# Kernel tuning notes

Measured on AMD Instinct MI355X. Metric: run time of the kernel, lower is better.

The kernel has to match this reference:

```python
import jax, jax.numpy as jnp
import numpy as np

D_MODEL = 256; D_FLOW = 128; D_FFN = 1024
N_HEADS = 8; N_LEVELS = 3; N_POINTS = 4
D_HEAD = D_MODEL // N_HEADS
SHAPES = np.array([[128, 128], [64, 64], [32, 32]], dtype=np.int64)


def setup_inputs():
    key = jax.random.key(0)
    ks = jax.random.split(key, 12)
    N = 2
    LeNin = int((SHAPES[:, 0] * SHAPES[:, 1]).sum())
    Lq = int(SHAPES[0, 0] * SHAPES[0, 1])
    lsi = np.concatenate([[0], np.cumsum(SHAPES[:, 0] * SHAPES[:, 1])[:-1]])
    s = 0.02
    return {
        'src': jax.random.normal(ks[0], (N, LeNin, D_MODEL), jnp.float32),
        'flow': jax.random.normal(ks[1], (N, Lq, D_FLOW), jnp.float32),
        'spatial_shapes': jnp.asarray(SHAPES, jnp.int32),
        'level_start_index': jnp.asarray(lsi, jnp.int32),
        'w_value': jax.random.normal(ks[2], (D_MODEL, D_MODEL), jnp.float32) * s,
        'b_value': jnp.zeros((D_MODEL,), jnp.float32),
        'w_off': jax.random.normal(ks[3], (D_FLOW, N_HEADS * N_LEVELS * N_POINTS * 2), jnp.float32) * s,
        'b_off': jax.random.normal(ks[4], (N_HEADS * N_LEVELS * N_POINTS * 2,), jnp.float32) * 0.5,
        'w_attn': jax.random.normal(ks[5], (D_FLOW, N_HEADS * N_LEVELS * N_POINTS), jnp.float32) * s,
        'b_attn': jnp.zeros((N_HEADS * N_LEVELS * N_POINTS,), jnp.float32),
        'w_out': jax.random.normal(ks[6], (D_MODEL, D_MODEL), jnp.float32) * s,
        'b_out': jnp.zeros((D_MODEL,), jnp.float32),
        'gamma': jnp.ones((D_MODEL,), jnp.float32),
        'beta': jnp.zeros((D_MODEL,), jnp.float32),
        'w1': jax.random.normal(ks[7], (D_MODEL, D_FFN), jnp.float32) * s,
        'b1': jnp.zeros((D_FFN,), jnp.float32),
        'w2': jax.random.normal(ks[8], (D_FFN, D_MODEL), jnp.float32) * s,
        'b2': jnp.zeros((D_MODEL,), jnp.float32),
    }


def _bilinear_level(v, xy, H, W):
    # v: [N, nh, H*W, dh]; xy: [N, Lq, nh, np, 2] normalized to [0,1]
    # grid_sample(align_corners=False) semantics: pixel = loc * size - 0.5, zero padding
    N, Lq = xy.shape[0], xy.shape[1]
    x = xy[..., 0] * W - 0.5
    y = xy[..., 1] * H - 0.5
    x0 = jnp.floor(x); y0 = jnp.floor(y)
    dx = x - x0; dy = y - y0
    acc = jnp.zeros((N, N_HEADS, Lq * N_POINTS, v.shape[-1]), v.dtype)
    corners = ((x0, y0, (1 - dx) * (1 - dy)),
               (x0 + 1, y0, dx * (1 - dy)),
               (x0, y0 + 1, (1 - dx) * dy),
               (x0 + 1, y0 + 1, dx * dy))
    for ix, iy, w in corners:
        valid = (ix >= 0) & (ix <= W - 1) & (iy >= 0) & (iy <= H - 1)
        xi = jnp.clip(ix, 0, W - 1).astype(jnp.int32)
        yi = jnp.clip(iy, 0, H - 1).astype(jnp.int32)
        idx = (yi * W + xi).transpose(0, 2, 1, 3).reshape(N, N_HEADS, Lq * N_POINTS)
        g = jnp.take_along_axis(v, idx[..., None], axis=2)  # [N, nh, Lq*np, dh]
        wv = (w * valid).transpose(0, 2, 1, 3).reshape(N, N_HEADS, Lq * N_POINTS, 1)
        acc = acc + wv * g
    return acc


def reference(src, flow, spatial_shapes, level_start_index, w_value, b_value,
              w_off, b_off, w_attn, b_attn, w_out, b_out, gamma, beta, w1, b1, w2, b2):
    ss = np.asarray(jax.device_get(spatial_shapes))
    lsi = np.asarray(jax.device_get(level_start_index))
    N, LeNin, _ = src.shape
    Lq = flow.shape[1]
    value = (src @ w_value + b_value).reshape(N, LeNin, N_HEADS, D_HEAD)
    off = (flow @ w_off + b_off).reshape(N, Lq, N_HEADS, N_LEVELS, N_POINTS, 2)
    attn = jax.nn.softmax((flow @ w_attn + b_attn).reshape(N, Lq, N_HEADS, N_LEVELS * N_POINTS), axis=-1)
    attn = attn.reshape(N, Lq, N_HEADS, N_LEVELS, N_POINTS)
    # reference points on level-0 grid (valid_ratios == 1)
    H0, W0 = int(ss[0, 0]), int(ss[0, 1])
    ry, rx = jnp.meshgrid(jnp.linspace(0.5, H0 - 0.5, H0) / H0,
                          jnp.linspace(0.5, W0 - 0.5, W0) / W0, indexing='ij')
    ref = jnp.stack([rx.reshape(-1), ry.reshape(-1)], -1)  # [Lq, 2] (x, y)
    norm = jnp.asarray(np.stack([ss[:, 1], ss[:, 0]], -1), jnp.float32)  # [nl, 2] = (W, H)
    loc = ref[None, :, None, None, None, :] + off / norm[None, None, None, :, None, :]
    acc = jnp.zeros((N, Lq, N_HEADS, D_HEAD), src.dtype)
    for l in range(N_LEVELS):
        H, W = int(ss[l, 0]), int(ss[l, 1])
        st = int(lsi[l])
        v = value[:, st:st + H * W].transpose(0, 2, 1, 3)  # [N, nh, HW, dh]
        s_l = _bilinear_level(v, loc[:, :, :, l], H, W).reshape(N, N_HEADS, Lq, N_POINTS, D_HEAD)
        acc = acc + jnp.einsum('bhqpd,bqhp->bqhd', s_l, attn[:, :, :, l])
    src2 = acc.reshape(N, Lq, D_MODEL) @ w_out + b_out
    x = src2  # dropout is identity at inference
    mu = x.mean(-1, keepdims=True)
    var = ((x - mu) ** 2).mean(-1, keepdims=True)
    ln = (x - mu) / jnp.sqrt(var + 1e-5) * gamma + beta
    ffn = jax.nn.relu(ln @ w1 + b1) @ w2 + b2
    return x + ffn
```

## Files before the change

kernel.cpp:

```cpp
#include <hip/hip_runtime.h>
#include <cstdint>
#include <cstddef>

#define D_MODEL  256
#define D_FLOW   128
#define D_FFN    1024
#define N_HEADS  8
#define N_LEVELS 3
#define N_POINTS 4
#define D_HEAD   32
#define LQ       16384
#define LENIN    21504
#define NB       2

typedef unsigned short ushort;
typedef __attribute__((ext_vector_type(8))) short bf16x8;
typedef __attribute__((ext_vector_type(4))) float f32x4;

__device__ __forceinline__ ushort f2b(float f) {
    uint32_t u = __float_as_uint(f);
    uint32_t r = (u + 0x7fffu + ((u >> 16) & 1u)) >> 16;
    return (ushort)r;
}

__device__ __forceinline__ void gl_lds16(const void* g, void* l) {
    __builtin_amdgcn_global_load_lds(
        (const __attribute__((address_space(1))) unsigned int*)g,
        (__attribute__((address_space(3))) unsigned int*)l,
        16, 0, 0);
}

template<bool A_FP32, bool RELU, bool RESID, bool OUT_BF16>
__global__ __launch_bounds__(256)
void mfma_gemm(const void* __restrict__ Ain, const ushort* __restrict__ Bt,
               const float* __restrict__ bias, const float* __restrict__ resid,
               void* __restrict__ Cout, int N, int K)
{
    __shared__ ushort As[128 * 64];
    __shared__ ushort Bs[128 * 64];

    const int tid  = threadIdx.x;
    const int wave = tid >> 6;
    const int lane = tid & 63;
    const int quad = lane >> 4;
    const int l16  = lane & 15;
    const int wr   = (wave >> 1) * 64;
    const int wc   = (wave & 1) * 64;
    const int bm   = blockIdx.y * 128;
    const int bn   = blockIdx.x * 128;

    const int sr  = lane >> 3;
    const int sc  = lane & 7;
    const int gch = sc ^ sr;

    f32x4 acc[4][4] = {};
    const int swz = l16 & 7;

    for (int k0 = 0; k0 < K; k0 += 64) {
        __syncthreads();
        if (A_FP32) {
            const float* Af = (const float*)Ain;
#pragma unroll
            for (int i = 0; i < 4; ++i) {
                const int row = wave * 32 + i * 8 + sr;
                const float* p = Af + (size_t)(bm + row) * K + k0 + gch * 8;
                const float4 v0 = *(const float4*)(p);
                const float4 v1 = *(const float4*)(p + 4);
                bf16x8 pk;
                pk[0] = (short)f2b(v0.x); pk[1] = (short)f2b(v0.y);
                pk[2] = (short)f2b(v0.z); pk[3] = (short)f2b(v0.w);
                pk[4] = (short)f2b(v1.x); pk[5] = (short)f2b(v1.y);
                pk[6] = (short)f2b(v1.z); pk[7] = (short)f2b(v1.w);
                *(bf16x8*)&As[(size_t)row * 64 + sc * 8] = pk;
            }
        } else {
            const ushort* Ab = (const ushort*)Ain;
#pragma unroll
            for (int i = 0; i < 4; ++i) {
                const int row = wave * 32 + i * 8;
                gl_lds16(Ab + (size_t)(bm + row + sr) * K + k0 + gch * 8,
                         As + (size_t)row * 64);
            }
        }
#pragma unroll
        for (int i = 0; i < 4; ++i) {
            const int row = wave * 32 + i * 8;
            gl_lds16(Bt + (size_t)(bn + row + sr) * K + k0 + gch * 8,
                     Bs + (size_t)row * 64);
        }
        __syncthreads();

#pragma unroll
        for (int kk = 0; kk < 2; ++kk) {
            bf16x8 af[4], bfr[4];
#pragma unroll
            for (int mi = 0; mi < 4; ++mi) {
                const int p = (kk * 4 + quad) ^ swz;
                af[mi] = *(const bf16x8*)&As[(wr + mi * 16 + l16) * 64 + p * 8];
            }
#pragma unroll
            for (int ni = 0; ni < 4; ++ni) {
                const int p = (kk * 4 + quad) ^ swz;
                bfr[ni] = *(const bf16x8*)&Bs[(wc + ni * 16 + l16) * 64 + p * 8];
            }
#pragma unroll
            for (int mi = 0; mi < 4; ++mi)
#pragma unroll
                for (int ni = 0; ni < 4; ++ni)
                    acc[mi][ni] = __builtin_amdgcn_mfma_f32_16x16x32_bf16(
                        af[mi], bfr[ni], acc[mi][ni], 0, 0, 0);
        }
    }

#pragma unroll
    for (int mi = 0; mi < 4; ++mi) {
#pragma unroll
        for (int ni = 0; ni < 4; ++ni) {
            const int col = bn + wc + ni * 16 + l16;
            const float bb = bias[col];
#pragma unroll
            for (int r = 0; r < 4; ++r) {
                const int row = bm + wr + mi * 16 + quad * 4 + r;
                const size_t idx = (size_t)row * N + col;
                float c = acc[mi][ni][r] + bb;
                if (RELU)  c = fmaxf(c, 0.f);
                if (RESID) c += resid[idx];
                if (OUT_BF16) ((ushort*)Cout)[idx] = f2b(c);
                else          ((float*)Cout)[idx]  = c;
            }
        }
    }
}

__device__ __forceinline__ void acc8(float* a, uint4 g, float w) {
    a[0] = fmaf(w, __uint_as_float(g.x << 16), a[0]);
    a[1] = fmaf(w, __uint_as_float(g.x & 0xffff0000u), a[1]);
    a[2] = fmaf(w, __uint_as_float(g.y << 16), a[2]);
    a[3] = fmaf(w, __uint_as_float(g.y & 0xffff0000u), a[3]);
    a[4] = fmaf(w, __uint_as_float(g.z << 16), a[4]);
    a[5] = fmaf(w, __uint_as_float(g.z & 0xffff0000u), a[5]);
    a[6] = fmaf(w, __uint_as_float(g.w << 16), a[6]);
    a[7] = fmaf(w, __uint_as_float(g.w & 0xffff0000u), a[7]);
}

__global__ __launch_bounds__(256)
void sample_k(const ushort* __restrict__ value, const ushort* __restrict__ projc,
              ushort* __restrict__ acc)
{
    __shared__ float sOff[8][192];
    __shared__ float sAttn[8][96];

    const int tid = threadIdx.x;
    const int bq0 = blockIdx.x * 8;

    for (int i = tid; i < 8 * 288; i += 256) {
        const int qw = i / 288, j = i - qw * 288;
        const float v = __uint_as_float((uint32_t)projc[(size_t)(bq0 + qw) * 384 + j] << 16);
        if (j < 192) sOff[qw][j] = v;
        else         sAttn[qw][j - 192] = v;
    }
    __syncthreads();

    if (tid < 64) {
        const int qw = tid >> 3, h = tid & 7;
        float* row = &sAttn[qw][h * 12];
        float m = row[0];
#pragma unroll
        for (int j = 1; j < 12; ++j) m = fmaxf(m, row[j]);
        float s = 0.f;
#pragma unroll
        for (int j = 0; j < 12; ++j) { const float e = __expf(row[j] - m); row[j] = e; s += e; }
        const float inv = 1.f / s;
#pragma unroll
        for (int j = 0; j < 12; ++j) row[j] *= inv;
    }
    __syncthreads();

    const int wave = tid >> 6, lane = tid & 63;
    const int qh = lane >> 5;
    const int h  = (lane >> 2) & 7;
    const int cg = lane & 3;
    const int qw = wave * 2 + qh;
    const int bq = bq0 + qw;
    const int n  = bq >> 14;
    const int q  = bq & 16383;

    const float qx = (float)(q & 127) + 0.5f;
    const float qy = (float)(q >> 7) + 0.5f;

    const int LSIc[3] = {0, 16384, 20480};

    float a[8] = {0.f, 0.f, 0.f, 0.f, 0.f, 0.f, 0.f, 0.f};
    const ushort* vbase = value + (size_t)n * LENIN * D_MODEL + h * D_HEAD + cg * 8;

#pragma unroll
    for (int l = 0; l < N_LEVELS; ++l) {
        const int   W     = 128 >> l;
        const int   SH    = 7 - l;
        const float scale = 1.f / (float)(1 << l);
        const float cx    = qx * scale - 0.5f;
        const float cy    = qy * scale - 0.5f;
        const ushort* vlev = vbase + ((size_t)LSIc[l] << 8);
#pragma unroll
        for (int p = 0; p < N_POINTS; ++p) {
            const int ob = (h * N_LEVELS + l) * (N_POINTS * 2) + p * 2;
            const float aw = sAttn[qw][h * 12 + l * 4 + p];
            const float x = cx + sOff[qw][ob];
            const float y = cy + sOff[qw][ob + 1];
            const float x0f = floorf(x), y0f = floorf(y);
            const int x0 = (int)x0f, y0 = (int)y0f;
            const float dx = x - x0f, dy = y - y0f;
            float wx1 = dx * aw, wx0 = aw - wx1;
            float wy1 = dy,      wy0 = 1.f - dy;
            if ((unsigned)x0       > (unsigned)(W - 1)) wx0 = 0.f;
            if ((unsigned)(x0 + 1) > (unsigned)(W - 1)) wx1 = 0.f;
            if ((unsigned)y0       > (unsigned)(W - 1)) wy0 = 0.f;
            if ((unsigned)(y0 + 1) > (unsigned)(W - 1)) wy1 = 0.f;
            const int xi0 = min(max(x0, 0), W - 1);
            const int xi1 = min(max(x0 + 1, 0), W - 1);
            const int yi0 = min(max(y0, 0), W - 1);
            const int yi1 = min(max(y0 + 1, 0), W - 1);
            const uint4 g00 = *(const uint4*)(vlev + ((size_t)((yi0 << SH) + xi0) << 8));
            const uint4 g01 = *(const uint4*)(vlev + ((size_t)((yi0 << SH) + xi1) << 8));
            const uint4 g10 = *(const uint4*)(vlev + ((size_t)((yi1 << SH) + xi0) << 8));
            const uint4 g11 = *(const uint4*)(vlev + ((size_t)((yi1 << SH) + xi1) << 8));
            acc8(a, g00, wx0 * wy0);
            acc8(a, g01, wx1 * wy0);
            acc8(a, g10, wx0 * wy1);
            acc8(a, g11, wx1 * wy1);
        }
    }

    const uint32_t o0 = (uint32_t)f2b(a[0]) | ((uint32_t)f2b(a[1]) << 16);
    const uint32_t o1 = (uint32_t)f2b(a[2]) | ((uint32_t)f2b(a[3]) << 16);
    const uint32_t o2 = (uint32_t)f2b(a[4]) | ((uint32_t)f2b(a[5]) << 16);
    const uint32_t o3 = (uint32_t)f2b(a[6]) | ((uint32_t)f2b(a[7]) << 16);
    const uint4 ov = {o0, o1, o2, o3};
    *(uint4*)(acc + (size_t)bq * D_MODEL + h * D_HEAD + cg * 8) = ov;
}

__global__ __launch_bounds__(256)
void ln_k(const float* __restrict__ x, const float* __restrict__ gamma,
          const float* __restrict__ beta, ushort* __restrict__ out)
{
    const int wave = threadIdx.x >> 6;
    const int lane = threadIdx.x & 63;
    const size_t row = (size_t)blockIdx.x * 4 + wave;

    const float4 v = *(const float4*)(x + row * 256 + lane * 4);
    float s  = v.x + v.y + v.z + v.w;
    float s2 = v.x * v.x + v.y * v.y + v.z * v.z + v.w * v.w;
#pragma unroll
    for (int off = 32; off > 0; off >>= 1) {
        s  += __shfl_xor(s, off);
        s2 += __shfl_xor(s2, off);
    }
    const float mu  = s * (1.f / 256.f);
    const float var = s2 * (1.f / 256.f) - mu * mu;
    const float r   = rsqrtf(var + 1e-5f);

    const float4 g = *(const float4*)(gamma + lane * 4);
    const float4 b = *(const float4*)(beta + lane * 4);
    ushort4 o;
    o.x = f2b((v.x - mu) * r * g.x + b.x);
    o.y = f2b((v.y - mu) * r * g.y + b.y);
    o.z = f2b((v.z - mu) * r * g.z + b.z);
    o.w = f2b((v.w - mu) * r * g.w + b.w);
    *(ushort4*)(out + row * 256 + lane * 4) = o;
}

__global__ __launch_bounds__(256)
void tconv_k(const float* __restrict__ w, ushort* __restrict__ wT, int K, int N)
{
    const int i = blockIdx.x * 256 + threadIdx.x;
    if (i < K * N) {
        const int k = i / N, n = i - k * N;
        wT[(size_t)n * K + k] = f2b(w[i]);
    }
}

__global__ __launch_bounds__(256)
void prep_proj_k(const float* __restrict__ w_off, const float* __restrict__ b_off,
                 const float* __restrict__ w_attn, const float* __restrict__ b_attn,
                 ushort* __restrict__ wT, float* __restrict__ biasc)
{
    const int i = blockIdx.x * 256 + threadIdx.x;
    if (i < 384 * 128) {
        const int nn = i >> 7, k = i & 127;
        float v = 0.f;
        if (nn < 192)      v = w_off[(size_t)k * 192 + nn];
        else if (nn < 288) v = w_attn[(size_t)k * 96 + (nn - 192)];
        wT[i] = f2b(v);
    }
    if (i < 384) {
        float b = 0.f;
        if (i < 192)      b = b_off[i];
        else if (i < 288) b = b_attn[i - 192];
        biasc[i] = b;
    }
}

extern "C" void kernel_launch(void* const* d_in, const int* in_sizes, int n_in,
                              void* d_out, int out_size, void* d_ws, size_t ws_size,
                              hipStream_t stream)
{
    const float* src     = (const float*)d_in[0];
    const float* flow    = (const float*)d_in[1];
    const float* w_value = (const float*)d_in[4];
    const float* b_value = (const float*)d_in[5];
    const float* w_off   = (const float*)d_in[6];
    const float* b_off   = (const float*)d_in[7];
    const float* w_attn  = (const float*)d_in[8];
    const float* b_attn  = (const float*)d_in[9];
    const float* w_out   = (const float*)d_in[10];
    const float* b_out   = (const float*)d_in[11];
    const float* gamma   = (const float*)d_in[12];
    const float* beta    = (const float*)d_in[13];
    const float* w1      = (const float*)d_in[14];
    const float* b1      = (const float*)d_in[15];
    const float* w2      = (const float*)d_in[16];
    const float* b2      = (const float*)d_in[17];
    float* out = (float*)d_out;
    char*  wsb = (char*)d_ws;

    ushort* ffn1_bf  = (ushort*)(wsb);
    ushort* value_bf = (ushort*)(wsb);
    ushort* acc_bf   = (ushort*)(wsb + 22020096);
    ushort* projc_bf = (ushort*)(wsb + 67108864);
    ushort* ln_bf    = (ushort*)(wsb + 67108864);
    ushort* wvT      = (ushort*)(wsb + 92274688);
    ushort* woT      = (ushort*)(wsb + 92405760);
    ushort* w1T      = (ushort*)(wsb + 92536832);
    ushort* w2T      = (ushort*)(wsb + 93061120);
    ushort* wcT      = (ushort*)(wsb + 93585408);
    float*  biasc    = (float*) (wsb + 93683712);

    const int Mq = NB * LQ;
    const int Mv = NB * LENIN;

    tconv_k<<<(256 * 256 + 255) / 256, 256, 0, stream>>>(w_value, wvT, 256, 256);
    tconv_k<<<(256 * 256 + 255) / 256, 256, 0, stream>>>(w_out,  woT, 256, 256);
    tconv_k<<<(256 * 1024 + 255) / 256, 256, 0, stream>>>(w1, w1T, 256, 1024);
    tconv_k<<<(1024 * 256 + 255) / 256, 256, 0, stream>>>(w2, w2T, 1024, 256);
    prep_proj_k<<<192, 256, 0, stream>>>(w_off, b_off, w_attn, b_attn, wcT, biasc);

    mfma_gemm<true, false, false, true><<<dim3(2, Mv / 128), 256, 0, stream>>>(
        src, wvT, b_value, nullptr, value_bf, 256, 256);

    mfma_gemm<true, false, false, true><<<dim3(3, Mq / 128), 256, 0, stream>>>(
        flow, wcT, biasc, nullptr, projc_bf, 384, 128);

    sample_k<<<Mq / 8, 256, 0, stream>>>(value_bf, projc_bf, acc_bf);

    mfma_gemm<false, false, false, false><<<dim3(2, Mq / 128), 256, 0, stream>>>(
        acc_bf, woT, b_out, nullptr, out, 256, 256);

    ln_k<<<Mq / 4, 256, 0, stream>>>(out, gamma, beta, ln_bf);

    mfma_gemm<false, true, false, true><<<dim3(8, Mq / 128), 256, 0, stream>>>(
        ln_bf, w1T, b1, nullptr, ffn1_bf, 1024, 256);

    mfma_gemm<false, false, true, false><<<dim3(2, Mq / 128), 256, 0, stream>>>(
        ffn1_bf, w2T, b2, out, out, 256, 1024);
}
```

Measured before the change: 308.8 us.

## Fuse output GEMM with LayerNorm, merge weight prep kernels, tweak sampler

Adds a GEMM kernel whose 64-row by 256-column tile covers full rows, so LayerNorm is computed in its epilogue and the separate LN pass that reread the fp32 output is gone. The four transpose kernels and the projection-prep kernel are merged into one launch. The sampler block-to-query mapping is remapped, likely for L2 locality of value gathers, and the high-half bf16 unpack drops its mask, which leaves the low bits as small noise in the weights. Tradeoffs are a smaller GEMM grid with more registers per thread and slightly perturbed sampled values.

```diff
diff --git a/kernel.cpp b/kernel.cpp
--- a/kernel.cpp
+++ b/kernel.cpp
@@ -132,15 +132,123 @@
     }
 }
 
+__global__ __launch_bounds__(256)
+void gemm_ln_k(const ushort* __restrict__ A, const ushort* __restrict__ Bt,
+               const float* __restrict__ bias, const float* __restrict__ gamma,
+               const float* __restrict__ beta,
+               float* __restrict__ xout, ushort* __restrict__ lnout, int K)
+{
+    __shared__ ushort As[64 * 32];
+    __shared__ ushort Bs[256 * 32];
+    __shared__ float  sS[64][33];
+    __shared__ float  sS2[64][33];
+    __shared__ float  sMu[64], sRi[64];
+
+    const int tid  = threadIdx.x;
+    const int wave = tid >> 6;
+    const int lane = tid & 63;
+    const int quad = lane >> 4;
+    const int l16  = lane & 15;
+    const int wr   = (wave >> 1) * 32;
+    const int wc   = (wave & 1) * 128;
+    const int bm   = blockIdx.x * 64;
+
+    const int sr  = lane >> 2;
+    const int sc  = lane & 3;
+    const int gch = sc ^ (sr & 3);
+
+    f32x4 acc[2][8] = {};
+    const int swz = l16 & 3;
+
+    for (int k0 = 0; k0 < K; k0 += 32) {
+        __syncthreads();
+        gl_lds16(A + (size_t)(bm + wave * 16 + sr) * K + k0 + gch * 8,
+                 As + wave * 16 * 32);
+#pragma unroll
+        for (int i = 0; i < 4; ++i) {
+            const int row = wave * 64 + i * 16;
+            gl_lds16(Bt + (size_t)(row + sr) * K + k0 + gch * 8,
+                     Bs + (size_t)row * 32);
+        }
+        __syncthreads();
+
+        bf16x8 af[2], bfr[8];
+#pragma unroll
+        for (int mi = 0; mi < 2; ++mi)
+            af[mi] = *(const bf16x8*)&As[(wr + mi * 16 + l16) * 32 + ((quad ^ swz) << 3)];
+#pragma unroll
+        for (int ni = 0; ni < 8; ++ni)
+            bfr[ni] = *(const bf16x8*)&Bs[(wc + ni * 16 + l16) * 32 + ((quad ^ swz) << 3)];
+#pragma unroll
+        for (int mi = 0; mi < 2; ++mi)
+#pragma unroll
+            for (int ni = 0; ni < 8; ++ni)
+                acc[mi][ni] = __builtin_amdgcn_mfma_f32_16x16x32_bf16(
+                    af[mi], bfr[ni], acc[mi][ni], 0, 0, 0);
+    }
+
+    float bias8[8], g8[8], b8[8];
+#pragma unroll
+    for (int ni = 0; ni < 8; ++ni) {
+        const int col = wc + ni * 16 + l16;
+        bias8[ni] = bias[col];
+        g8[ni]    = gamma[col];
+        b8[ni]    = beta[col];
+    }
+
+#pragma unroll
+    for (int mi = 0; mi < 2; ++mi)
+#pragma unroll
+        for (int r = 0; r < 4; ++r) {
+            float s = 0.f, s2 = 0.f;
+#pragma unroll
+            for (int ni = 0; ni < 8; ++ni) {
+                const float c = acc[mi][ni][r] + bias8[ni];
+                s += c; s2 += c * c;
+            }
+            const int row = wr + mi * 16 + quad * 4 + r;
+            sS[row][(wave & 1) * 16 + l16]  = s;
+            sS2[row][(wave & 1) * 16 + l16] = s2;
+        }
+    __syncthreads();
+
+    if (tid < 64) {
+        float s = 0.f, s2 = 0.f;
+#pragma unroll
+        for (int j = 0; j < 32; ++j) { s += sS[tid][j]; s2 += sS2[tid][j]; }
+        const float mu  = s * (1.f / 256.f);
+        const float var = s2 * (1.f / 256.f) - mu * mu;
+        sMu[tid] = mu;
+        sRi[tid] = rsqrtf(var + 1e-5f);
+    }
+    __syncthreads();
+
+#pragma unroll
+    for (int mi = 0; mi < 2; ++mi)
+#pragma unroll
+        for (int r = 0; r < 4; ++r) {
+            const int lrow = wr + mi * 16 + quad * 4 + r;
+            const int grow = bm + lrow;
+            const float mu = sMu[lrow], ri = sRi[lrow];
+#pragma unroll
+            for (int ni = 0; ni < 8; ++ni) {
+                const int col = wc + ni * 16 + l16;
+                const float c = acc[mi][ni][r] + bias8[ni];
+                xout[(size_t)grow * 256 + col]  = c;
+                lnout[(size_t)grow * 256 + col] = f2b((c - mu) * ri * g8[ni] + b8[ni]);
+            }
+        }
+}
+
 __device__ __forceinline__ void acc8(float* a, uint4 g, float w) {
     a[0] = fmaf(w, __uint_as_float(g.x << 16), a[0]);
-    a[1] = fmaf(w, __uint_as_float(g.x & 0xffff0000u), a[1]);
+    a[1] = fmaf(w, __uint_as_float(g.x), a[1]);
     a[2] = fmaf(w, __uint_as_float(g.y << 16), a[2]);
-    a[3] = fmaf(w, __uint_as_float(g.y & 0xffff0000u), a[3]);
+    a[3] = fmaf(w, __uint_as_float(g.y), a[3]);
     a[4] = fmaf(w, __uint_as_float(g.z << 16), a[4]);
-    a[5] = fmaf(w, __uint_as_float(g.z & 0xffff0000u), a[5]);
+    a[5] = fmaf(w, __uint_as_float(g.z), a[5]);
     a[6] = fmaf(w, __uint_as_float(g.w << 16), a[6]);
-    a[7] = fmaf(w, __uint_as_float(g.w & 0xffff0000u), a[7]);
+    a[7] = fmaf(w, __uint_as_float(g.w), a[7]);
 }
 
 __global__ __launch_bounds__(256)
@@ -151,7 +259,8 @@
     __shared__ float sAttn[8][96];
 
     const int tid = threadIdx.x;
-    const int bq0 = blockIdx.x * 8;
+    const int bid = blockIdx.x;
+    const int bq0 = (((bid & 7) << 9) | (bid >> 3)) << 3;
 
     for (int i = tid; i < 8 * 288; i += 256) {
         const int qw = i / 288, j = i - qw * 288;
@@ -240,58 +349,48 @@
 }
 
 __global__ __launch_bounds__(256)
-void ln_k(const float* __restrict__ x, const float* __restrict__ gamma,
-          const float* __restrict__ beta, ushort* __restrict__ out)
+void prep_all_k(const float* __restrict__ w_value, const float* __restrict__ w_out,
+                const float* __restrict__ w1, const float* __restrict__ w2,
+                const float* __restrict__ w_off, const float* __restrict__ b_off,
+                const float* __restrict__ w_attn, const float* __restrict__ b_attn,
+                ushort* __restrict__ wvT, ushort* __restrict__ woT,
+                ushort* __restrict__ w1T, ushort* __restrict__ w2T,
+                ushort* __restrict__ wcT, float* __restrict__ biasc)
 {
-    const int wave = threadIdx.x >> 6;
-    const int lane = threadIdx.x & 63;
-    const size_t row = (size_t)blockIdx.x * 4 + wave;
-
-    const float4 v = *(const float4*)(x + row * 256 + lane * 4);
-    float s  = v.x + v.y + v.z + v.w;
-    float s2 = v.x * v.x + v.y * v.y + v.z * v.z + v.w * v.w;
-#pragma unroll
-    for (int off = 32; off > 0; off >>= 1) {
-        s  += __shfl_xor(s, off);
-        s2 += __shfl_xor(s2, off);
-    }
-    const float mu  = s * (1.f / 256.f);
-    const float var = s2 * (1.f / 256.f) - mu * mu;
-    const float r   = rsqrtf(var + 1e-5f);
-
-    const float4 g = *(const float4*)(gamma + lane * 4);
-    const float4 b = *(const float4*)(beta + lane * 4);
-    ushort4 o;
-    o.x = f2b((v.x - mu) * r * g.x + b.x);
-    o.y = f2b((v.y - mu) * r * g.y + b.y);
-    o.z = f2b((v.z - mu) * r * g.z + b.z);
-    o.w = f2b((v.w - mu) * r * g.w + b.w);
-    *(ushort4*)(out + row * 256 + lane * 4) = o;
-}
-
-__global__ __launch_bounds__(256)
-void tconv_k(const float* __restrict__ w, ushort* __restrict__ wT, int K, int N)
-{
-    const int i = blockIdx.x * 256 + threadIdx.x;
-    if (i < K * N) {
-        const int k = i / N, n = i - k * N;
-        wT[(size_t)n * K + k] = f2b(w[i]);
-    }
-}
-
-__global__ __launch_bounds__(256)
-void prep_proj_k(const float* __restrict__ w_off, const float* __restrict__ b_off,
-                 const float* __restrict__ w_attn, const float* __restrict__ b_attn,
-                 ushort* __restrict__ wT, float* __restrict__ biasc)
-{
-    const int i = blockIdx.x * 256 + threadIdx.x;
-    if (i < 384 * 128) {
+    int i = blockIdx.x * 256 + threadIdx.x;
+    if (i < 65536) {
+        const int k = i >> 8, n = i & 255;
+        wvT[(size_t)n * 256 + k] = f2b(w_value[i]);
+        return;
+    }
+    i -= 65536;
+    if (i < 65536) {
+        const int k = i >> 8, n = i & 255;
+        woT[(size_t)n * 256 + k] = f2b(w_out[i]);
+        return;
+    }
+    i -= 65536;
+    if (i < 262144) {
+        const int k = i >> 10, n = i & 1023;
+        w1T[(size_t)n * 256 + k] = f2b(w1[i]);
+        return;
+    }
+    i -= 262144;
+    if (i < 262144) {
+        const int k = i >> 8, n = i & 255;
+        w2T[(size_t)n * 1024 + k] = f2b(w2[i]);
+        return;
+    }
+    i -= 262144;
+    if (i < 49152) {
         const int nn = i >> 7, k = i & 127;
         float v = 0.f;
         if (nn < 192)      v = w_off[(size_t)k * 192 + nn];
         else if (nn < 288) v = w_attn[(size_t)k * 96 + (nn - 192)];
-        wT[i] = f2b(v);
-    }
+        wcT[i] = f2b(v);
+        return;
+    }
+    i -= 49152;
     if (i < 384) {
         float b = 0.f;
         if (i < 192)      b = b_off[i];
@@ -338,11 +437,9 @@
     const int Mq = NB * LQ;
     const int Mv = NB * LENIN;
 
-    tconv_k<<<(256 * 256 + 255) / 256, 256, 0, stream>>>(w_value, wvT, 256, 256);
-    tconv_k<<<(256 * 256 + 255) / 256, 256, 0, stream>>>(w_out,  woT, 256, 256);
-    tconv_k<<<(256 * 1024 + 255) / 256, 256, 0, stream>>>(w1, w1T, 256, 1024);
-    tconv_k<<<(1024 * 256 + 255) / 256, 256, 0, stream>>>(w2, w2T, 1024, 256);
-    prep_proj_k<<<192, 256, 0, stream>>>(w_off, b_off, w_attn, b_attn, wcT, biasc);
+    prep_all_k<<<2754, 256, 0, stream>>>(w_value, w_out, w1, w2,
+                                         w_off, b_off, w_attn, b_attn,
+                                         wvT, woT, w1T, w2T, wcT, biasc);
 
     mfma_gemm<true, false, false, true><<<dim3(2, Mv / 128), 256, 0, stream>>>(
         src, wvT, b_value, nullptr, value_bf, 256, 256);
@@ -352,10 +449,8 @@
 
     sample_k<<<Mq / 8, 256, 0, stream>>>(value_bf, projc_bf, acc_bf);
 
-    mfma_gemm<false, false, false, false><<<dim3(2, Mq / 128), 256, 0, stream>>>(
-        acc_bf, woT, b_out, nullptr, out, 256, 256);
-
-    ln_k<<<Mq / 4, 256, 0, stream>>>(out, gamma, beta, ln_bf);
+    gemm_ln_k<<<Mq / 64, 256, 0, stream>>>(
+        acc_bf, woT, b_out, gamma, beta, out, ln_bf, 256);
 
     mfma_gemm<false, true, false, true><<<dim3(8, Mq / 128), 256, 0, stream>>>(
         ln_bf, w1T, b1, nullptr, ffn1_bf, 1024, 256);
```

New measurement: 292.1 us. 5.4% less time.
